# Kernel tuning notes

Hardware: AMD Instinct MI355X
Metric: run time of the kernel (lower is better)

Reference implementation:

```python
import jax, jax.numpy as jnp
import numpy as np

N, D = 4096, 512
TAU, ALPHA, BETA = 0.8, 0.55, 0.4
ADJ_P = 0.005  # sparse binary adjacency density (avg degree ~20)


def setup_inputs() -> dict:
    key = jax.random.key(0)
    ks = jax.random.split(key, 8)
    z1 = jax.random.normal(ks[0], (N, D), dtype=jnp.float32)
    z2 = jax.random.normal(ks[1], (N, D), dtype=jnp.float32)

    def adj(k):
        a = jax.random.bernoulli(k, ADJ_P, (N, N)).astype(jnp.float32)
        # adjacency masks are binary {0,1}; zero the diagonal like the model does
        return a * (1.0 - jnp.eye(N, dtype=jnp.float32))

    return {
        "z1": z1,
        "z2": z2,
        "adj_c": adj(ks[2]),
        "adj_m": adj(ks[3]),
        "adj_f": adj(ks[4]),
        "adj_c_aug": adj(ks[5]),
        "adj_m_aug": adj(ks[6]),
        "adj_f_aug": adj(ks[7]),
    }


def _normalize(z):
    # F.normalize(z, dim=1): divide by L2 norm clamped at 1e-12
    n = jnp.maximum(jnp.linalg.norm(z, axis=1, keepdims=True), 1e-12)
    return z / n


def _cl_loss(z, z_aug, adj, tau):
    zn = _normalize(z)
    zan = _normalize(z_aug)
    intra = jnp.exp((zn @ zn.T) / tau)          # [N, N]
    inter = jnp.exp((zn @ zan.T) / tau)         # [N, N]
    intra_diag = jnp.diagonal(intra)
    positive = jnp.diagonal(inter) + (intra * adj).sum(1) + (inter * adj).sum(1)
    denom = intra.sum(1) + inter.sum(1) - intra_diag
    adj_count = adj.sum(1) * 2.0 + 1.0
    loss = jnp.log(positive / denom) / adj_count
    return -jnp.mean(loss)


def _final_cl_loss(z, z_aug, adj, adj_aug, tau):
    return ALPHA * _cl_loss(z, z_aug, adj, tau) + BETA * _cl_loss(z_aug, z, adj_aug, tau)


def reference(z1, z2, adj_c, adj_m, adj_f, adj_c_aug, adj_m_aug, adj_f_aug):
    loss_coarse = _final_cl_loss(z1, z2, adj_c, adj_c_aug, TAU)
    loss_medium = _final_cl_loss(z1, z2, adj_m, adj_m_aug, TAU)
    loss_fine = _final_cl_loss(z1, z2, adj_f, adj_f_aug, TAU)
    loss_cross_cf = _final_cl_loss(z1, z2, adj_c, adj_f_aug, TAU * 0.8)
    loss_cross_mf = _final_cl_loss(z1, z2, adj_m, adj_f_aug, TAU * 0.9)

    sc, sm, sf = adj_c.sum(), adj_m.sum(), adj_f.sum()
    total_info = sc + sm + sf + 1e-08
    scale_loss = (sc / total_info) * loss_coarse + (sm / total_info) * loss_medium + (sf / total_info) * loss_fine
    cross_loss = 0.2 * (loss_cross_cf + loss_cross_mf)
    return scale_loss + cross_loss
```

## Files before the change

### kernel.cpp

```cpp
#include <hip/hip_runtime.h>
#include <hip/hip_bf16.h>

#define NR 4096
#define DD 512
#define CAP 64

typedef __bf16 bf16x8 __attribute__((ext_vector_type(8)));
typedef float f32x4 __attribute__((ext_vector_type(4)));
typedef unsigned short u16;

#define AS_GLOBAL(p) ((const __attribute__((address_space(1))) unsigned int*)(p))
#define AS_LDS(p)    ((__attribute__((address_space(3))) unsigned int*)(p))

__device__ __forceinline__ u16 f2bf(float x) {
    __hip_bfloat16 h = __float2bfloat16(x);
    return *reinterpret_cast<u16*>(&h);
}

__device__ __forceinline__ float blo(unsigned u) { return __uint_as_float(u << 16); }
__device__ __forceinline__ float bhi(unsigned u) { return __uint_as_float(u & 0xffff0000u); }

__global__ void norm_kernel(const float* z1, const float* z2,
                            u16* zn1, u16* zn2, float* d12) {
    const int row = blockIdx.x;
    const int t = threadIdx.x;
    const float* r1 = z1 + (size_t)row * DD;
    const float* r2 = z2 + (size_t)row * DD;
    float a0 = r1[t], a1 = r1[t + 256];
    float b0 = r2[t], b1 = r2[t + 256];
    float ss1 = a0 * a0 + a1 * a1;
    float ss2 = b0 * b0 + b1 * b1;
    #pragma unroll
    for (int m = 1; m < 64; m <<= 1) {
        ss1 += __shfl_xor(ss1, m);
        ss2 += __shfl_xor(ss2, m);
    }
    __shared__ float s1s[4], s2s[4], ds[4];
    const int wid = t >> 6, lane = t & 63;
    if (lane == 0) { s1s[wid] = ss1; s2s[wid] = ss2; }
    __syncthreads();
    const float n1 = s1s[0] + s1s[1] + s1s[2] + s1s[3];
    const float n2 = s2s[0] + s2s[1] + s2s[2] + s2s[3];
    const float inv1 = 1.0f / fmaxf(sqrtf(n1), 1e-12f);
    const float inv2 = 1.0f / fmaxf(sqrtf(n2), 1e-12f);
    const float u0 = a0 * inv1, u1 = a1 * inv1;
    const float v0 = b0 * inv2, v1 = b1 * inv2;
    zn1[(size_t)row * DD + t]       = f2bf(u0);
    zn1[(size_t)row * DD + t + 256] = f2bf(u1);
    zn2[(size_t)row * DD + t]       = f2bf(v0);
    zn2[(size_t)row * DD + t + 256] = f2bf(v1);
    float dp = u0 * v0 + u1 * v1;
    #pragma unroll
    for (int m = 1; m < 64; m <<= 1) dp += __shfl_xor(dp, m);
    if (lane == 0) ds[wid] = dp;
    __syncthreads();
    if (t == 0) d12[row] = ds[0] + ds[1] + ds[2] + ds[3];
}

__global__ __launch_bounds__(256)
void sparsify_kernel(const float* m0, const float* m1, const float* m2,
                     const float* m3, const float* m4, const float* m5,
                     int* cnts, int* idx, float* asum) {
    const int row = blockIdx.x;
    const int m = blockIdx.y;
    const int t = threadIdx.x;
    const float* M = (m == 0) ? m0 : (m == 1) ? m1 : (m == 2) ? m2
                   : (m == 3) ? m3 : (m == 4) ? m4 : m5;
    const float* rowp = M + (size_t)row * NR;
    __shared__ int s_cnt;
    __shared__ int s_idx[CAP];
    if (t == 0) s_cnt = 0;
    __syncthreads();
    #pragma unroll
    for (int q = 0; q < 4; q++) {
        const int vi = t + 256 * q;
        const float4 v = ((const float4*)rowp)[vi];
        const int col = vi * 4;
        if (v.x != 0.f) { int p = atomicAdd(&s_cnt, 1); if (p < CAP) s_idx[p] = col; }
        if (v.y != 0.f) { int p = atomicAdd(&s_cnt, 1); if (p < CAP) s_idx[p] = col + 1; }
        if (v.z != 0.f) { int p = atomicAdd(&s_cnt, 1); if (p < CAP) s_idx[p] = col + 2; }
        if (v.w != 0.f) { int p = atomicAdd(&s_cnt, 1); if (p < CAP) s_idx[p] = col + 3; }
    }
    __syncthreads();
    const int c = min(s_cnt, CAP);
    const size_t base = (size_t)m * NR + row;
    if (t < c) idx[base * CAP + t] = s_idx[t];
    if (t == 0) { cnts[base] = c; asum[base] = (float)s_cnt; }
}

__global__ __launch_bounds__(256, 3)
void score_kernel(const u16* __restrict__ zn1, const u16* __restrict__ zn2,
                  float* __restrict__ part) {
    int id = blockIdx.x;
    int mode, by, bx;
    if (id < 1024) {
        mode = 1; by = id >> 5; bx = id & 31;
    } else {
        int k = id - 1024;
        mode = 0;
        if (k >= 528) { k -= 528; mode = 2; }
        int v = (int)((65.0f - sqrtf(4225.0f - 8.0f * (float)k)) * 0.5f);
        if (v < 0) v = 0; if (v > 31) v = 31;
        while (v < 31 && (v + 1) * 32 - ((v + 1) * v) / 2 <= k) v++;
        while (v > 0 && v * 32 - (v * (v - 1)) / 2 > k) v--;
        by = v;
        bx = by + (k - (by * 32 - (by * (by - 1)) / 2));
    }
    const int Ib = by * 128, Jb = bx * 128;
    const u16* Ag = (mode == 2) ? zn2 : zn1;
    const u16* Bg = (mode == 0) ? zn1 : zn2;
    const int p_row = mode;
    const int p_col = (mode == 1) ? 3 : mode;
    const bool do_cols = (mode == 1) || (bx != by);

    __shared__ u16 As[128 * 64];
    __shared__ u16 Bs[128 * 64];
    __shared__ float sRow[2][3][128];
    __shared__ float sCol[2][3][128];

    const int tid = threadIdx.x;
    const int lane = tid & 63;
    const int wid = tid >> 6;
    const int wm = wid >> 1, wn = wid & 1;
    const int quad = lane >> 4, lcol = lane & 15;

    f32x4 acc[4][4];
    #pragma unroll
    for (int a = 0; a < 4; a++)
        #pragma unroll
        for (int b = 0; b < 4; b++)
            acc[a][b] = (f32x4){0.f, 0.f, 0.f, 0.f};

    size_t gA[4], gB[4];
    unsigned ldsoff[4];
    #pragma unroll
    for (int cc = 0; cc < 4; cc++) {
        const int ch = cc * 4 + wid;
        const int p = ch * 64 + lane;
        const int r = p >> 3;
        const int kb = (p & 7) ^ (r & 7);
        ldsoff[cc] = (unsigned)ch * 1024u;
        gA[cc] = (size_t)(Ib + r) * DD + kb * 8;
        gB[cc] = (size_t)(Jb + r) * DD + kb * 8;
    }

    for (int k0 = 0; k0 < DD; k0 += 64) {
        __syncthreads();
        #pragma unroll
        for (int cc = 0; cc < 4; cc++) {
            __builtin_amdgcn_global_load_lds(AS_GLOBAL(Ag + gA[cc] + k0),
                                             AS_LDS((char*)As + ldsoff[cc]), 16, 0, 0);
            __builtin_amdgcn_global_load_lds(AS_GLOBAL(Bg + gB[cc] + k0),
                                             AS_LDS((char*)Bs + ldsoff[cc]), 16, 0, 0);
        }
        __syncthreads();
        #pragma unroll
        for (int kk = 0; kk < 64; kk += 32) {
            const int kbb = (kk >> 3) + quad;
            bf16x8 a[4], b[4];
            #pragma unroll
            for (int i = 0; i < 4; i++) {
                const int ra = wm * 64 + i * 16 + lcol;
                const int rb = wn * 64 + i * 16 + lcol;
                a[i] = *(const bf16x8*)&As[ra * 64 + ((kbb ^ (ra & 7)) * 8)];
                b[i] = *(const bf16x8*)&Bs[rb * 64 + ((kbb ^ (rb & 7)) * 8)];
            }
            #pragma unroll
            for (int mi = 0; mi < 4; mi++)
                #pragma unroll
                for (int ni = 0; ni < 4; ni++)
                    acc[mi][ni] = __builtin_amdgcn_mfma_f32_16x16x32_bf16(a[mi], b[ni], acc[mi][ni], 0, 0, 0);
        }
    }

    const float C0 = 1.8033688011112042f;
    const float C1 = 2.2542110013890054f;
    const float C2 = 2.0037431123457825f;

    float colacc[3][4];
    #pragma unroll
    for (int t = 0; t < 3; t++)
        #pragma unroll
        for (int ni = 0; ni < 4; ni++) colacc[t][ni] = 0.f;

    #pragma unroll
    for (int mi = 0; mi < 4; mi++) {
        #pragma unroll
        for (int reg = 0; reg < 4; reg++) {
            float p0 = 0.f, p1 = 0.f, p2 = 0.f;
            #pragma unroll
            for (int ni = 0; ni < 4; ni++) {
                const float s = acc[mi][ni][reg];
                const float e0 = __builtin_amdgcn_exp2f(s * C0);
                const float e1 = __builtin_amdgcn_exp2f(s * C1);
                const float e2 = __builtin_amdgcn_exp2f(s * C2);
                p0 += e0; p1 += e1; p2 += e2;
                colacc[0][ni] += e0; colacc[1][ni] += e1; colacc[2][ni] += e2;
            }
            p0 += __shfl_xor(p0, 1); p0 += __shfl_xor(p0, 2); p0 += __shfl_xor(p0, 4); p0 += __shfl_xor(p0, 8);
            p1 += __shfl_xor(p1, 1); p1 += __shfl_xor(p1, 2); p1 += __shfl_xor(p1, 4); p1 += __shfl_xor(p1, 8);
            p2 += __shfl_xor(p2, 1); p2 += __shfl_xor(p2, 2); p2 += __shfl_xor(p2, 4); p2 += __shfl_xor(p2, 8);
            if (lcol == 0) {
                const int r = wm * 64 + mi * 16 + quad * 4 + reg;
                sRow[wn][0][r] = p0; sRow[wn][1][r] = p1; sRow[wn][2][r] = p2;
            }
        }
    }
    #pragma unroll
    for (int t = 0; t < 3; t++) {
        #pragma unroll
        for (int ni = 0; ni < 4; ni++) {
            float v = colacc[t][ni];
            v += __shfl_xor(v, 16); v += __shfl_xor(v, 32);
            if (quad == 0) sCol[wm][t][wn * 64 + ni * 16 + lcol] = v;
        }
    }
    __syncthreads();
    if (tid < 128) {
        const int i = Ib + tid;
        #pragma unroll
        for (int t = 0; t < 3; t++) {
            const float v = sRow[0][t][tid] + sRow[1][t][tid];
            part[(((size_t)p_row * 3 + t) * 32 + bx) * NR + i] = v;
        }
    } else if (do_cols) {
        const int c = tid - 128;
        const int i = Jb + c;
        #pragma unroll
        for (int t = 0; t < 3; t++) {
            const float v = sCol[0][t][c] + sCol[1][t][c];
            part[(((size_t)p_col * 3 + t) * 32 + by) * NR + i] = v;
        }
    }
}

__global__ __launch_bounds__(256)
void reduce_kernel(const float* __restrict__ part, float* __restrict__ rs) {
    const int g = blockIdx.x * 256 + threadIdx.x;
    const int pt = g >> 12;
    const int i = g & (NR - 1);
    const float* base = part + ((size_t)pt * 32) * NR + i;
    float s = 0.f;
    #pragma unroll
    for (int k = 0; k < 32; k++) s += base[(size_t)k * NR];
    rs[(size_t)pt * NR + i] = s;
}

__global__ __launch_bounds__(256)
void sparse_kernel(const u16* __restrict__ zn1, const u16* __restrict__ zn2,
                   const int* __restrict__ cnts, const int* __restrict__ idx,
                   float* __restrict__ ms) {
    const int w = blockIdx.x * 4 + (threadIdx.x >> 6);
    const int lane = threadIdx.x & 63;
    const int g = lane >> 4;
    const int l = lane & 15;
    const int m = w >> 12;
    const int i = w & (NR - 1);

    const float C0 = 1.8033688011112042f;
    const float C1 = 2.2542110013890054f;
    const float C2 = 2.0037431123457825f;

    int nslot; int slot[3]; float coef[3];
    switch (m) {
        case 0: nslot = 2; slot[0] = 0; coef[0] = C0; slot[1] = 3; coef[1] = C1; break;
        case 1: nslot = 2; slot[0] = 1; coef[0] = C0; slot[1] = 4; coef[1] = C2; break;
        case 2: nslot = 1; slot[0] = 2; coef[0] = C0; break;
        case 3: nslot = 1; slot[0] = 0; coef[0] = C0; break;
        case 4: nslot = 1; slot[0] = 1; coef[0] = C0; break;
        default: nslot = 3; slot[0] = 2; coef[0] = C0; slot[1] = 3; coef[1] = C1;
                 slot[2] = 4; coef[2] = C2; break;
    }

    const u16* A = (m < 3) ? zn1 : zn2;
    float a[32];
    {
        const uint4* ap = (const uint4*)(A + (size_t)i * DD) + l * 4;
        #pragma unroll
        for (int t = 0; t < 4; t++) {
            const uint4 r = ap[t];
            const unsigned* u = (const unsigned*)&r;
            #pragma unroll
            for (int q = 0; q < 4; q++) {
                a[t * 8 + 2 * q]     = blo(u[q]);
                a[t * 8 + 2 * q + 1] = bhi(u[q]);
            }
        }
    }

    const size_t base = (size_t)m * NR + i;
    const int cnt = cnts[base];
    const int* ji = idx + base * CAP;
    const int jreg = ji[(lane < cnt) ? lane : (cnt > 0 ? cnt - 1 : 0)];

    float acc[3][2] = {{0.f, 0.f}, {0.f, 0.f}, {0.f, 0.f}};

    for (int q0 = 0; q0 < cnt; q0 += 8) {
        const int qa = q0 + g;
        const int qb = qa + 4;
        const bool va = qa < cnt;
        const bool vb = qb < cnt;
        const int ja = __shfl(jreg, va ? qa : 0);
        const int jb = __shfl(jreg, vb ? qb : 0);

        const uint4* p1a = (const uint4*)(zn1 + (size_t)ja * DD) + l * 4;
        const uint4* p2a = (const uint4*)(zn2 + (size_t)ja * DD) + l * 4;
        const uint4* p1b = (const uint4*)(zn1 + (size_t)jb * DD) + l * 4;
        const uint4* p2b = (const uint4*)(zn2 + (size_t)jb * DD) + l * 4;
        uint4 r1a[4], r2a[4], r1b[4], r2b[4];
        #pragma unroll
        for (int t = 0; t < 4; t++) {
            r1a[t] = p1a[t]; r2a[t] = p2a[t];
            r1b[t] = p1b[t]; r2b[t] = p2b[t];
        }

        float s1a0 = 0.f, s1a1 = 0.f, s2a0 = 0.f, s2a1 = 0.f;
        float s1b0 = 0.f, s1b1 = 0.f, s2b0 = 0.f, s2b1 = 0.f;
        #pragma unroll
        for (int t = 0; t < 4; t++) {
            const unsigned* u1a = (const unsigned*)&r1a[t];
            const unsigned* u2a = (const unsigned*)&r2a[t];
            const unsigned* u1b = (const unsigned*)&r1b[t];
            const unsigned* u2b = (const unsigned*)&r2b[t];
            #pragma unroll
            for (int q = 0; q < 4; q++) {
                const float alo = a[t * 8 + 2 * q], ahi = a[t * 8 + 2 * q + 1];
                s1a0 += alo * blo(u1a[q]); s1a1 += ahi * bhi(u1a[q]);
                s2a0 += alo * blo(u2a[q]); s2a1 += ahi * bhi(u2a[q]);
                s1b0 += alo * blo(u1b[q]); s1b1 += ahi * bhi(u1b[q]);
                s2b0 += alo * blo(u2b[q]); s2b1 += ahi * bhi(u2b[q]);
            }
        }
        float d1a = s1a0 + s1a1, d2a = s2a0 + s2a1;
        float d1b = s1b0 + s1b1, d2b = s2b0 + s2b1;

        #pragma unroll
        for (int msk = 1; msk < 16; msk <<= 1) {
            d1a += __shfl_xor(d1a, msk); d2a += __shfl_xor(d2a, msk);
            d1b += __shfl_xor(d1b, msk); d2b += __shfl_xor(d2b, msk);
        }

        const float e1a = (m < 3) ? d1a : d2a, e2a = (m < 3) ? d2a : d1a;
        const float e1b = (m < 3) ? d1b : d2b, e2b = (m < 3) ? d2b : d1b;
        if (va) {
            for (int s = 0; s < nslot; s++) {
                acc[s][0] += __builtin_amdgcn_exp2f(e1a * coef[s]);
                acc[s][1] += __builtin_amdgcn_exp2f(e2a * coef[s]);
            }
        }
        if (vb) {
            for (int s = 0; s < nslot; s++) {
                acc[s][0] += __builtin_amdgcn_exp2f(e1b * coef[s]);
                acc[s][1] += __builtin_amdgcn_exp2f(e2b * coef[s]);
            }
        }
    }

    #pragma unroll
    for (int s = 0; s < 3; s++) {
        #pragma unroll
        for (int h = 0; h < 2; h++) {
            float v = acc[s][h];
            v += __shfl_xor(v, 16);
            v += __shfl_xor(v, 32);
            acc[s][h] = v;
        }
    }
    if (lane == 0) {
        const int pb = (m < 3) ? 0 : 2;
        for (int s = 0; s < nslot; s++) {
            ms[((pb)     * 5 + slot[s]) * NR + i] = acc[s][0];
            ms[((pb + 1) * 5 + slot[s]) * NR + i] = acc[s][1];
        }
    }
}

__global__ void finalize_kernel(const float* rs, const float* ms, const float* asum,
                                const float* d12, float* out) {
    const int t = threadIdx.x;
    const int tA[5] = {0, 0, 0, 1, 2};
    const int kA[5] = {0, 1, 2, 3, 4};
    const int aA[5] = {0, 1, 2, 0, 1};
    const int aB[5] = {3, 4, 5, 5, 5};
    const float it[3] = {1.25f, 1.5625f, 1.3888888888888888f};
    const float e1t[3] = {expf(1.25f), expf(1.5625f), expf(1.3888888888888888f)};

    float LA[5] = {0, 0, 0, 0, 0}, LB[5] = {0, 0, 0, 0, 0};
    float sc = 0.f, sm = 0.f, sf = 0.f;

    for (int i = t; i < NR; i += 256) {
        const float d = d12[i];
        float ed[3];
        ed[0] = __expf(d * it[0]); ed[1] = __expf(d * it[1]); ed[2] = __expf(d * it[2]);
        float R[4][3], M[4][5], A6[6];
        #pragma unroll
        for (int p = 0; p < 4; p++) {
            #pragma unroll
            for (int tt = 0; tt < 3; tt++) R[p][tt] = rs[(p * 3 + tt) * NR + i];
            #pragma unroll
            for (int k = 0; k < 5; k++) M[p][k] = ms[(p * 5 + k) * NR + i];
        }
        #pragma unroll
        for (int a = 0; a < 6; a++) A6[a] = asum[a * NR + i];

        #pragma unroll
        for (int c = 0; c < 5; c++) {
            const int tt = tA[c], k = kA[c];
            float pos = ed[tt] + M[0][k] + M[1][k];
            float den = R[0][tt] + R[1][tt] - e1t[tt];
            float cnt = 2.f * A6[aA[c]] + 1.f;
            LA[c] += __logf(pos / den) / cnt;
            pos = ed[tt] + M[2][k] + M[3][k];
            den = R[2][tt] + R[3][tt] - e1t[tt];
            cnt = 2.f * A6[aB[c]] + 1.f;
            LB[c] += __logf(pos / den) / cnt;
        }
        sc += A6[0]; sm += A6[1]; sf += A6[2];
    }

    __shared__ float red[256];
    float vals[13] = {LA[0], LA[1], LA[2], LA[3], LA[4],
                      LB[0], LB[1], LB[2], LB[3], LB[4], sc, sm, sf};
    __shared__ float tot[13];
    for (int q = 0; q < 13; q++) {
        red[t] = vals[q];
        __syncthreads();
        for (int s = 128; s > 0; s >>= 1) {
            if (t < s) red[t] += red[t + s];
            __syncthreads();
        }
        if (t == 0) tot[q] = red[0];
        __syncthreads();
    }
    if (t == 0) {
        float Ac[5], Bc[5];
        #pragma unroll
        for (int c = 0; c < 5; c++) {
            Ac[c] = -tot[c] / (float)NR;
            Bc[c] = -tot[5 + c] / (float)NR;
        }
        const float ALPHA = 0.55f, BETA = 0.4f;
        const float Lc  = ALPHA * Ac[0] + BETA * Bc[0];
        const float Lm  = ALPHA * Ac[1] + BETA * Bc[1];
        const float Lf  = ALPHA * Ac[2] + BETA * Bc[2];
        const float Lcf = ALPHA * Ac[3] + BETA * Bc[3];
        const float Lmf = ALPHA * Ac[4] + BETA * Bc[4];
        const float scs = tot[10], sms = tot[11], sfs = tot[12];
        const float tot_info = scs + sms + sfs + 1e-8f;
        out[0] = (scs * Lc + sms * Lm + sfs * Lf) / tot_info + 0.2f * (Lcf + Lmf);
    }
}

extern "C" void kernel_launch(void* const* d_in, const int* in_sizes, int n_in,
                              void* d_out, int out_size, void* d_ws, size_t ws_size,
                              hipStream_t stream) {
    const float* z1  = (const float*)d_in[0];
    const float* z2  = (const float*)d_in[1];
    const float* ac  = (const float*)d_in[2];
    const float* am  = (const float*)d_in[3];
    const float* af  = (const float*)d_in[4];
    const float* aca = (const float*)d_in[5];
    const float* ama = (const float*)d_in[6];
    const float* afa = (const float*)d_in[7];

    float* ws   = (float*)d_ws;
    float* rs   = ws;
    float* ms   = rs + 12 * NR;
    float* asum = ms + 20 * NR;
    float* d12  = asum + 6 * NR;
    u16* zn1 = (u16*)(d12 + NR);
    u16* zn2 = zn1 + (size_t)NR * DD;
    int* cnts = (int*)(zn2 + (size_t)NR * DD);
    int* idx  = cnts + 6 * NR;
    float* part = (float*)(idx + (size_t)6 * NR * CAP);

    norm_kernel<<<NR, 256, 0, stream>>>(z1, z2, zn1, zn2, d12);
    dim3 sg(NR, 6);
    sparsify_kernel<<<sg, 256, 0, stream>>>(ac, am, af, aca, ama, afa, cnts, idx, asum);
    score_kernel<<<1024 + 2 * 528, 256, 0, stream>>>(zn1, zn2, part);
    sparse_kernel<<<6 * NR / 4, 256, 0, stream>>>(zn1, zn2, cnts, idx, ms);
    reduce_kernel<<<12 * NR / 256, 256, 0, stream>>>(part, rs);
    finalize_kernel<<<1, 256, 0, stream>>>(rs, ms, asum, d12, (float*)d_out);
}
```

Measured before the change: 585.5 us.

## Fuse dense score and sparse neighbor kernels; wave-per-row sparsify with ballot-free scan

```diff
diff --git a/kernel.cpp b/kernel.cpp
--- a/kernel.cpp
+++ b/kernel.cpp
@@ -61,175 +61,315 @@
 void sparsify_kernel(const float* m0, const float* m1, const float* m2,
                      const float* m3, const float* m4, const float* m5,
                      int* cnts, int* idx, float* asum) {
-    const int row = blockIdx.x;
-    const int m = blockIdx.y;
-    const int t = threadIdx.x;
+    const int w = blockIdx.x * 4 + (threadIdx.x >> 6);
+    const int lane = threadIdx.x & 63;
+    const int m = w >> 12;
+    const int row = w & (NR - 1);
     const float* M = (m == 0) ? m0 : (m == 1) ? m1 : (m == 2) ? m2
                    : (m == 3) ? m3 : (m == 4) ? m4 : m5;
-    const float* rowp = M + (size_t)row * NR;
-    __shared__ int s_cnt;
-    __shared__ int s_idx[CAP];
-    if (t == 0) s_cnt = 0;
-    __syncthreads();
+    const float4* p = (const float4*)(M + (size_t)row * NR) + lane;
+
+    unsigned long long mask = 0ull;
     #pragma unroll
-    for (int q = 0; q < 4; q++) {
-        const int vi = t + 256 * q;
-        const float4 v = ((const float4*)rowp)[vi];
-        const int col = vi * 4;
-        if (v.x != 0.f) { int p = atomicAdd(&s_cnt, 1); if (p < CAP) s_idx[p] = col; }
-        if (v.y != 0.f) { int p = atomicAdd(&s_cnt, 1); if (p < CAP) s_idx[p] = col + 1; }
-        if (v.z != 0.f) { int p = atomicAdd(&s_cnt, 1); if (p < CAP) s_idx[p] = col + 2; }
-        if (v.w != 0.f) { int p = atomicAdd(&s_cnt, 1); if (p < CAP) s_idx[p] = col + 3; }
-    }
-    __syncthreads();
-    const int c = min(s_cnt, CAP);
+    for (int t = 0; t < 16; t++) {
+        const float4 v = p[t * 64];
+        mask |= (unsigned long long)((v.x != 0.f ? 1u : 0u)
+               | (v.y != 0.f ? 2u : 0u)
+               | (v.z != 0.f ? 4u : 0u)
+               | (v.w != 0.f ? 8u : 0u)) << (t * 4);
+    }
+    const int n = __popcll(mask);
+    int off = n;
+    #pragma unroll
+    for (int d = 1; d < 64; d <<= 1) {
+        const int tu = __shfl_up(off, d);
+        if (lane >= d) off += tu;
+    }
+    const int total = __shfl(off, 63);
+    int pos = off - n;
     const size_t base = (size_t)m * NR + row;
-    if (t < c) idx[base * CAP + t] = s_idx[t];
-    if (t == 0) { cnts[base] = c; asum[base] = (float)s_cnt; }
-}
-
-__global__ __launch_bounds__(256, 3)
-void score_kernel(const u16* __restrict__ zn1, const u16* __restrict__ zn2,
-                  float* __restrict__ part) {
-    int id = blockIdx.x;
-    int mode, by, bx;
-    if (id < 1024) {
-        mode = 1; by = id >> 5; bx = id & 31;
-    } else {
-        int k = id - 1024;
-        mode = 0;
-        if (k >= 528) { k -= 528; mode = 2; }
-        int v = (int)((65.0f - sqrtf(4225.0f - 8.0f * (float)k)) * 0.5f);
-        if (v < 0) v = 0; if (v > 31) v = 31;
-        while (v < 31 && (v + 1) * 32 - ((v + 1) * v) / 2 <= k) v++;
-        while (v > 0 && v * 32 - (v * (v - 1)) / 2 > k) v--;
-        by = v;
-        bx = by + (k - (by * 32 - (by * (by - 1)) / 2));
-    }
-    const int Ib = by * 128, Jb = bx * 128;
-    const u16* Ag = (mode == 2) ? zn2 : zn1;
-    const u16* Bg = (mode == 0) ? zn1 : zn2;
-    const int p_row = mode;
-    const int p_col = (mode == 1) ? 3 : mode;
-    const bool do_cols = (mode == 1) || (bx != by);
-
+    unsigned long long mm = mask;
+    while (mm) {
+        const int b = __ffsll(mm) - 1;
+        mm &= mm - 1;
+        const int t = b >> 2, j = b & 3;
+        if (pos < CAP) idx[base * CAP + pos] = (t * 64 + lane) * 4 + j;
+        pos++;
+    }
+    if (lane == 63) {
+        cnts[base] = min(total, CAP);
+        asum[base] = (float)total;
+    }
+}
+
+__global__ __launch_bounds__(256, 4)
+void fused_kernel(const u16* __restrict__ zn1, const u16* __restrict__ zn2,
+                  const int* __restrict__ cnts, const int* __restrict__ idx,
+                  float* __restrict__ part, float* __restrict__ ms) {
     __shared__ u16 As[128 * 64];
     __shared__ u16 Bs[128 * 64];
     __shared__ float sRow[2][3][128];
     __shared__ float sCol[2][3][128];
 
+    const int bid = blockIdx.x;
     const int tid = threadIdx.x;
     const int lane = tid & 63;
-    const int wid = tid >> 6;
-    const int wm = wid >> 1, wn = wid & 1;
-    const int quad = lane >> 4, lcol = lane & 15;
-
-    f32x4 acc[4][4];
-    #pragma unroll
-    for (int a = 0; a < 4; a++)
-        #pragma unroll
-        for (int b = 0; b < 4; b++)
-            acc[a][b] = (f32x4){0.f, 0.f, 0.f, 0.f};
-
-    size_t gA[4], gB[4];
-    unsigned ldsoff[4];
-    #pragma unroll
-    for (int cc = 0; cc < 4; cc++) {
-        const int ch = cc * 4 + wid;
-        const int p = ch * 64 + lane;
-        const int r = p >> 3;
-        const int kb = (p & 7) ^ (r & 7);
-        ldsoff[cc] = (unsigned)ch * 1024u;
-        gA[cc] = (size_t)(Ib + r) * DD + kb * 8;
-        gB[cc] = (size_t)(Jb + r) * DD + kb * 8;
-    }
-
-    for (int k0 = 0; k0 < DD; k0 += 64) {
-        __syncthreads();
-        #pragma unroll
-        for (int cc = 0; cc < 4; cc++) {
-            __builtin_amdgcn_global_load_lds(AS_GLOBAL(Ag + gA[cc] + k0),
-                                             AS_LDS((char*)As + ldsoff[cc]), 16, 0, 0);
-            __builtin_amdgcn_global_load_lds(AS_GLOBAL(Bg + gB[cc] + k0),
-                                             AS_LDS((char*)Bs + ldsoff[cc]), 16, 0, 0);
-        }
-        __syncthreads();
-        #pragma unroll
-        for (int kk = 0; kk < 64; kk += 32) {
-            const int kbb = (kk >> 3) + quad;
-            bf16x8 a[4], b[4];
-            #pragma unroll
-            for (int i = 0; i < 4; i++) {
-                const int ra = wm * 64 + i * 16 + lcol;
-                const int rb = wn * 64 + i * 16 + lcol;
-                a[i] = *(const bf16x8*)&As[ra * 64 + ((kbb ^ (ra & 7)) * 8)];
-                b[i] = *(const bf16x8*)&Bs[rb * 64 + ((kbb ^ (rb & 7)) * 8)];
-            }
-            #pragma unroll
-            for (int mi = 0; mi < 4; mi++)
-                #pragma unroll
-                for (int ni = 0; ni < 4; ni++)
-                    acc[mi][ni] = __builtin_amdgcn_mfma_f32_16x16x32_bf16(a[mi], b[ni], acc[mi][ni], 0, 0, 0);
-        }
-    }
 
     const float C0 = 1.8033688011112042f;
     const float C1 = 2.2542110013890054f;
     const float C2 = 2.0037431123457825f;
 
-    float colacc[3][4];
-    #pragma unroll
-    for (int t = 0; t < 3; t++)
-        #pragma unroll
-        for (int ni = 0; ni < 4; ni++) colacc[t][ni] = 0.f;
-
-    #pragma unroll
-    for (int mi = 0; mi < 4; mi++) {
-        #pragma unroll
-        for (int reg = 0; reg < 4; reg++) {
-            float p0 = 0.f, p1 = 0.f, p2 = 0.f;
+    if ((bid & 3) == 0) {
+        int id = bid >> 2;
+        int mode, by, bx;
+        if (id < 1024) {
+            mode = 1; by = id >> 5; bx = id & 31;
+        } else {
+            int k = id - 1024;
+            mode = 0;
+            if (k >= 528) { k -= 528; mode = 2; }
+            int v = (int)((65.0f - sqrtf(4225.0f - 8.0f * (float)k)) * 0.5f);
+            if (v < 0) v = 0; if (v > 31) v = 31;
+            while (v < 31 && (v + 1) * 32 - ((v + 1) * v) / 2 <= k) v++;
+            while (v > 0 && v * 32 - (v * (v - 1)) / 2 > k) v--;
+            by = v;
+            bx = by + (k - (by * 32 - (by * (by - 1)) / 2));
+        }
+        const int Ib = by * 128, Jb = bx * 128;
+        const u16* Ag = (mode == 2) ? zn2 : zn1;
+        const u16* Bg = (mode == 0) ? zn1 : zn2;
+        const int p_row = mode;
+        const int p_col = (mode == 1) ? 3 : mode;
+        const bool do_cols = (mode == 1) || (bx != by);
+
+        const int wid = tid >> 6;
+        const int wm = wid >> 1, wn = wid & 1;
+        const int quad = lane >> 4, lcol = lane & 15;
+
+        f32x4 acc[4][4];
+        #pragma unroll
+        for (int a = 0; a < 4; a++)
+            #pragma unroll
+            for (int b = 0; b < 4; b++)
+                acc[a][b] = (f32x4){0.f, 0.f, 0.f, 0.f};
+
+        size_t gA[4], gB[4];
+        unsigned ldsoff[4];
+        #pragma unroll
+        for (int cc = 0; cc < 4; cc++) {
+            const int ch = cc * 4 + wid;
+            const int p = ch * 64 + lane;
+            const int r = p >> 3;
+            const int kb = (p & 7) ^ (r & 7);
+            ldsoff[cc] = (unsigned)ch * 1024u;
+            gA[cc] = (size_t)(Ib + r) * DD + kb * 8;
+            gB[cc] = (size_t)(Jb + r) * DD + kb * 8;
+        }
+
+        for (int k0 = 0; k0 < DD; k0 += 64) {
+            __syncthreads();
+            #pragma unroll
+            for (int cc = 0; cc < 4; cc++) {
+                __builtin_amdgcn_global_load_lds(AS_GLOBAL(Ag + gA[cc] + k0),
+                                                 AS_LDS((char*)As + ldsoff[cc]), 16, 0, 0);
+                __builtin_amdgcn_global_load_lds(AS_GLOBAL(Bg + gB[cc] + k0),
+                                                 AS_LDS((char*)Bs + ldsoff[cc]), 16, 0, 0);
+            }
+            __syncthreads();
+            #pragma unroll
+            for (int kk = 0; kk < 64; kk += 32) {
+                const int kbb = (kk >> 3) + quad;
+                bf16x8 a[4], b[4];
+                #pragma unroll
+                for (int i = 0; i < 4; i++) {
+                    const int ra = wm * 64 + i * 16 + lcol;
+                    const int rb = wn * 64 + i * 16 + lcol;
+                    a[i] = *(const bf16x8*)&As[ra * 64 + ((kbb ^ (ra & 7)) * 8)];
+                    b[i] = *(const bf16x8*)&Bs[rb * 64 + ((kbb ^ (rb & 7)) * 8)];
+                }
+                #pragma unroll
+                for (int mi = 0; mi < 4; mi++)
+                    #pragma unroll
+                    for (int ni = 0; ni < 4; ni++)
+                        acc[mi][ni] = __builtin_amdgcn_mfma_f32_16x16x32_bf16(a[mi], b[ni], acc[mi][ni], 0, 0, 0);
+            }
+        }
+
+        float colacc[3][4];
+        #pragma unroll
+        for (int t = 0; t < 3; t++)
+            #pragma unroll
+            for (int ni = 0; ni < 4; ni++) colacc[t][ni] = 0.f;
+
+        #pragma unroll
+        for (int mi = 0; mi < 4; mi++) {
+            #pragma unroll
+            for (int reg = 0; reg < 4; reg++) {
+                float p0 = 0.f, p1 = 0.f, p2 = 0.f;
+                #pragma unroll
+                for (int ni = 0; ni < 4; ni++) {
+                    const float s = acc[mi][ni][reg];
+                    const float e0 = __builtin_amdgcn_exp2f(s * C0);
+                    const float e1 = __builtin_amdgcn_exp2f(s * C1);
+                    const float e2 = __builtin_amdgcn_exp2f(s * C2);
+                    p0 += e0; p1 += e1; p2 += e2;
+                    colacc[0][ni] += e0; colacc[1][ni] += e1; colacc[2][ni] += e2;
+                }
+                p0 += __shfl_xor(p0, 1); p0 += __shfl_xor(p0, 2); p0 += __shfl_xor(p0, 4); p0 += __shfl_xor(p0, 8);
+                p1 += __shfl_xor(p1, 1); p1 += __shfl_xor(p1, 2); p1 += __shfl_xor(p1, 4); p1 += __shfl_xor(p1, 8);
+                p2 += __shfl_xor(p2, 1); p2 += __shfl_xor(p2, 2); p2 += __shfl_xor(p2, 4); p2 += __shfl_xor(p2, 8);
+                if (lcol == 0) {
+                    const int r = wm * 64 + mi * 16 + quad * 4 + reg;
+                    sRow[wn][0][r] = p0; sRow[wn][1][r] = p1; sRow[wn][2][r] = p2;
+                }
+            }
+        }
+        #pragma unroll
+        for (int t = 0; t < 3; t++) {
             #pragma unroll
             for (int ni = 0; ni < 4; ni++) {
-                const float s = acc[mi][ni][reg];
-                const float e0 = __builtin_amdgcn_exp2f(s * C0);
-                const float e1 = __builtin_amdgcn_exp2f(s * C1);
-                const float e2 = __builtin_amdgcn_exp2f(s * C2);
-                p0 += e0; p1 += e1; p2 += e2;
-                colacc[0][ni] += e0; colacc[1][ni] += e1; colacc[2][ni] += e2;
-            }
-            p0 += __shfl_xor(p0, 1); p0 += __shfl_xor(p0, 2); p0 += __shfl_xor(p0, 4); p0 += __shfl_xor(p0, 8);
-            p1 += __shfl_xor(p1, 1); p1 += __shfl_xor(p1, 2); p1 += __shfl_xor(p1, 4); p1 += __shfl_xor(p1, 8);
-            p2 += __shfl_xor(p2, 1); p2 += __shfl_xor(p2, 2); p2 += __shfl_xor(p2, 4); p2 += __shfl_xor(p2, 8);
-            if (lcol == 0) {
-                const int r = wm * 64 + mi * 16 + quad * 4 + reg;
-                sRow[wn][0][r] = p0; sRow[wn][1][r] = p1; sRow[wn][2][r] = p2;
-            }
-        }
-    }
-    #pragma unroll
-    for (int t = 0; t < 3; t++) {
-        #pragma unroll
-        for (int ni = 0; ni < 4; ni++) {
-            float v = colacc[t][ni];
-            v += __shfl_xor(v, 16); v += __shfl_xor(v, 32);
-            if (quad == 0) sCol[wm][t][wn * 64 + ni * 16 + lcol] = v;
-        }
-    }
-    __syncthreads();
-    if (tid < 128) {
-        const int i = Ib + tid;
-        #pragma unroll
-        for (int t = 0; t < 3; t++) {
-            const float v = sRow[0][t][tid] + sRow[1][t][tid];
-            part[(((size_t)p_row * 3 + t) * 32 + bx) * NR + i] = v;
-        }
-    } else if (do_cols) {
-        const int c = tid - 128;
-        const int i = Jb + c;
-        #pragma unroll
-        for (int t = 0; t < 3; t++) {
-            const float v = sCol[0][t][c] + sCol[1][t][c];
-            part[(((size_t)p_col * 3 + t) * 32 + by) * NR + i] = v;
+                float v = colacc[t][ni];
+                v += __shfl_xor(v, 16); v += __shfl_xor(v, 32);
+                if (quad == 0) sCol[wm][t][wn * 64 + ni * 16 + lcol] = v;
+            }
+        }
+        __syncthreads();
+        if (tid < 128) {
+            const int i = Ib + tid;
+            #pragma unroll
+            for (int t = 0; t < 3; t++) {
+                const float v = sRow[0][t][tid] + sRow[1][t][tid];
+                part[(((size_t)p_row * 3 + t) * 32 + bx) * NR + i] = v;
+            }
+        } else if (do_cols) {
+            const int c = tid - 128;
+            const int i = Jb + c;
+            #pragma unroll
+            for (int t = 0; t < 3; t++) {
+                const float v = sCol[0][t][c] + sCol[1][t][c];
+                part[(((size_t)p_col * 3 + t) * 32 + by) * NR + i] = v;
+            }
+        }
+    } else {
+        const int sid = bid - (bid >> 2) - 1;
+        if (sid >= 6144) return;
+        const int w = sid * 4 + (tid >> 6);
+        const int g = lane >> 4;
+        const int l = lane & 15;
+        const int m = w >> 12;
+        const int i = w & (NR - 1);
+
+        int nslot; int slot[3]; float coef[3];
+        switch (m) {
+            case 0: nslot = 2; slot[0] = 0; coef[0] = C0; slot[1] = 3; coef[1] = C1; break;
+            case 1: nslot = 2; slot[0] = 1; coef[0] = C0; slot[1] = 4; coef[1] = C2; break;
+            case 2: nslot = 1; slot[0] = 2; coef[0] = C0; break;
+            case 3: nslot = 1; slot[0] = 0; coef[0] = C0; break;
+            case 4: nslot = 1; slot[0] = 1; coef[0] = C0; break;
+            default: nslot = 3; slot[0] = 2; coef[0] = C0; slot[1] = 3; coef[1] = C1;
+                     slot[2] = 4; coef[2] = C2; break;
+        }
+
+        const u16* A = (m < 3) ? zn1 : zn2;
+        float a[32];
+        {
+            const uint4* ap = (const uint4*)(A + (size_t)i * DD) + l * 4;
+            #pragma unroll
+            for (int t = 0; t < 4; t++) {
+                const uint4 r = ap[t];
+                const unsigned* u = (const unsigned*)&r;
+                #pragma unroll
+                for (int q = 0; q < 4; q++) {
+                    a[t * 8 + 2 * q]     = blo(u[q]);
+                    a[t * 8 + 2 * q + 1] = bhi(u[q]);
+                }
+            }
+        }
+
+        const size_t base = (size_t)m * NR + i;
+        const int cnt = cnts[base];
+        const int* ji = idx + base * CAP;
+        const int jreg = ji[(lane < cnt) ? lane : (cnt > 0 ? cnt - 1 : 0)];
+
+        float acc[3][2] = {{0.f, 0.f}, {0.f, 0.f}, {0.f, 0.f}};
+
+        for (int q0 = 0; q0 < cnt; q0 += 8) {
+            const int qa = q0 + g;
+            const int qb = qa + 4;
+            const bool va = qa < cnt;
+            const bool vb = qb < cnt;
+            const int ja = __shfl(jreg, va ? qa : 0);
+            const int jb = __shfl(jreg, vb ? qb : 0);
+
+            const uint4* p1a = (const uint4*)(zn1 + (size_t)ja * DD) + l * 4;
+            const uint4* p2a = (const uint4*)(zn2 + (size_t)ja * DD) + l * 4;
+            const uint4* p1b = (const uint4*)(zn1 + (size_t)jb * DD) + l * 4;
+            const uint4* p2b = (const uint4*)(zn2 + (size_t)jb * DD) + l * 4;
+            uint4 r1a[4], r2a[4], r1b[4], r2b[4];
+            #pragma unroll
+            for (int t = 0; t < 4; t++) {
+                r1a[t] = p1a[t]; r2a[t] = p2a[t];
+                r1b[t] = p1b[t]; r2b[t] = p2b[t];
+            }
+
+            float s1a0 = 0.f, s1a1 = 0.f, s2a0 = 0.f, s2a1 = 0.f;
+            float s1b0 = 0.f, s1b1 = 0.f, s2b0 = 0.f, s2b1 = 0.f;
+            #pragma unroll
+            for (int t = 0; t < 4; t++) {
+                const unsigned* u1a = (const unsigned*)&r1a[t];
+                const unsigned* u2a = (const unsigned*)&r2a[t];
+                const unsigned* u1b = (const unsigned*)&r1b[t];
+                const unsigned* u2b = (const unsigned*)&r2b[t];
+                #pragma unroll
+                for (int q = 0; q < 4; q++) {
+                    const float alo = a[t * 8 + 2 * q], ahi = a[t * 8 + 2 * q + 1];
+                    s1a0 += alo * blo(u1a[q]); s1a1 += ahi * bhi(u1a[q]);
+                    s2a0 += alo * blo(u2a[q]); s2a1 += ahi * bhi(u2a[q]);
+                    s1b0 += alo * blo(u1b[q]); s1b1 += ahi * bhi(u1b[q]);
+                    s2b0 += alo * blo(u2b[q]); s2b1 += ahi * bhi(u2b[q]);
+                }
+            }
+            float d1a = s1a0 + s1a1, d2a = s2a0 + s2a1;
+            float d1b = s1b0 + s1b1, d2b = s2b0 + s2b1;
+
+            #pragma unroll
+            for (int msk = 1; msk < 16; msk <<= 1) {
+                d1a += __shfl_xor(d1a, msk); d2a += __shfl_xor(d2a, msk);
+                d1b += __shfl_xor(d1b, msk); d2b += __shfl_xor(d2b, msk);
+            }
+
+            const float e1a = (m < 3) ? d1a : d2a, e2a = (m < 3) ? d2a : d1a;
+            const float e1b = (m < 3) ? d1b : d2b, e2b = (m < 3) ? d2b : d1b;
+            if (va) {
+                for (int s = 0; s < nslot; s++) {
+                    acc[s][0] += __builtin_amdgcn_exp2f(e1a * coef[s]);
+                    acc[s][1] += __builtin_amdgcn_exp2f(e2a * coef[s]);
+                }
+            }
+            if (vb) {
+                for (int s = 0; s < nslot; s++) {
+                    acc[s][0] += __builtin_amdgcn_exp2f(e1b * coef[s]);
+                    acc[s][1] += __builtin_amdgcn_exp2f(e2b * coef[s]);
+                }
+            }
+        }
+
+        #pragma unroll
+        for (int s = 0; s < 3; s++) {
+            #pragma unroll
+            for (int h = 0; h < 2; h++) {
+                float v = acc[s][h];
+                v += __shfl_xor(v, 16);
+                v += __shfl_xor(v, 32);
+                acc[s][h] = v;
+            }
+        }
+        if (lane == 0) {
+            const int pb = (m < 3) ? 0 : 2;
+            for (int s = 0; s < nslot; s++) {
+                ms[((pb)     * 5 + slot[s]) * NR + i] = acc[s][0];
+                ms[((pb + 1) * 5 + slot[s]) * NR + i] = acc[s][1];
+            }
         }
     }
 }
@@ -244,135 +384,6 @@
     #pragma unroll
     for (int k = 0; k < 32; k++) s += base[(size_t)k * NR];
     rs[(size_t)pt * NR + i] = s;
-}
-
-__global__ __launch_bounds__(256)
-void sparse_kernel(const u16* __restrict__ zn1, const u16* __restrict__ zn2,
-                   const int* __restrict__ cnts, const int* __restrict__ idx,
-                   float* __restrict__ ms) {
-    const int w = blockIdx.x * 4 + (threadIdx.x >> 6);
-    const int lane = threadIdx.x & 63;
-    const int g = lane >> 4;
-    const int l = lane & 15;
-    const int m = w >> 12;
-    const int i = w & (NR - 1);
-
-    const float C0 = 1.8033688011112042f;
-    const float C1 = 2.2542110013890054f;
-    const float C2 = 2.0037431123457825f;
-
-    int nslot; int slot[3]; float coef[3];
-    switch (m) {
-        case 0: nslot = 2; slot[0] = 0; coef[0] = C0; slot[1] = 3; coef[1] = C1; break;
-        case 1: nslot = 2; slot[0] = 1; coef[0] = C0; slot[1] = 4; coef[1] = C2; break;
-        case 2: nslot = 1; slot[0] = 2; coef[0] = C0; break;
-        case 3: nslot = 1; slot[0] = 0; coef[0] = C0; break;
-        case 4: nslot = 1; slot[0] = 1; coef[0] = C0; break;
-        default: nslot = 3; slot[0] = 2; coef[0] = C0; slot[1] = 3; coef[1] = C1;
-                 slot[2] = 4; coef[2] = C2; break;
-    }
-
-    const u16* A = (m < 3) ? zn1 : zn2;
-    float a[32];
-    {
-        const uint4* ap = (const uint4*)(A + (size_t)i * DD) + l * 4;
-        #pragma unroll
-        for (int t = 0; t < 4; t++) {
-            const uint4 r = ap[t];
-            const unsigned* u = (const unsigned*)&r;
-            #pragma unroll
-            for (int q = 0; q < 4; q++) {
-                a[t * 8 + 2 * q]     = blo(u[q]);
-                a[t * 8 + 2 * q + 1] = bhi(u[q]);
-            }
-        }
-    }
-
-    const size_t base = (size_t)m * NR + i;
-    const int cnt = cnts[base];
-    const int* ji = idx + base * CAP;
-    const int jreg = ji[(lane < cnt) ? lane : (cnt > 0 ? cnt - 1 : 0)];
-
-    float acc[3][2] = {{0.f, 0.f}, {0.f, 0.f}, {0.f, 0.f}};
-
-    for (int q0 = 0; q0 < cnt; q0 += 8) {
-        const int qa = q0 + g;
-        const int qb = qa + 4;
-        const bool va = qa < cnt;
-        const bool vb = qb < cnt;
-        const int ja = __shfl(jreg, va ? qa : 0);
-        const int jb = __shfl(jreg, vb ? qb : 0);
-
-        const uint4* p1a = (const uint4*)(zn1 + (size_t)ja * DD) + l * 4;
-        const uint4* p2a = (const uint4*)(zn2 + (size_t)ja * DD) + l * 4;
-        const uint4* p1b = (const uint4*)(zn1 + (size_t)jb * DD) + l * 4;
-        const uint4* p2b = (const uint4*)(zn2 + (size_t)jb * DD) + l * 4;
-        uint4 r1a[4], r2a[4], r1b[4], r2b[4];
-        #pragma unroll
-        for (int t = 0; t < 4; t++) {
-            r1a[t] = p1a[t]; r2a[t] = p2a[t];
-            r1b[t] = p1b[t]; r2b[t] = p2b[t];
-        }
-
-        float s1a0 = 0.f, s1a1 = 0.f, s2a0 = 0.f, s2a1 = 0.f;
-        float s1b0 = 0.f, s1b1 = 0.f, s2b0 = 0.f, s2b1 = 0.f;
-        #pragma unroll
-        for (int t = 0; t < 4; t++) {
-            const unsigned* u1a = (const unsigned*)&r1a[t];
-            const unsigned* u2a = (const unsigned*)&r2a[t];
-            const unsigned* u1b = (const unsigned*)&r1b[t];
-            const unsigned* u2b = (const unsigned*)&r2b[t];
-            #pragma unroll
-            for (int q = 0; q < 4; q++) {
-                const float alo = a[t * 8 + 2 * q], ahi = a[t * 8 + 2 * q + 1];
-                s1a0 += alo * blo(u1a[q]); s1a1 += ahi * bhi(u1a[q]);
-                s2a0 += alo * blo(u2a[q]); s2a1 += ahi * bhi(u2a[q]);
-                s1b0 += alo * blo(u1b[q]); s1b1 += ahi * bhi(u1b[q]);
-                s2b0 += alo * blo(u2b[q]); s2b1 += ahi * bhi(u2b[q]);
-            }
-        }
-        float d1a = s1a0 + s1a1, d2a = s2a0 + s2a1;
-        float d1b = s1b0 + s1b1, d2b = s2b0 + s2b1;
-
-        #pragma unroll
-        for (int msk = 1; msk < 16; msk <<= 1) {
-            d1a += __shfl_xor(d1a, msk); d2a += __shfl_xor(d2a, msk);
-            d1b += __shfl_xor(d1b, msk); d2b += __shfl_xor(d2b, msk);
-        }
-
-        const float e1a = (m < 3) ? d1a : d2a, e2a = (m < 3) ? d2a : d1a;
-        const float e1b = (m < 3) ? d1b : d2b, e2b = (m < 3) ? d2b : d1b;
-        if (va) {
-            for (int s = 0; s < nslot; s++) {
-                acc[s][0] += __builtin_amdgcn_exp2f(e1a * coef[s]);
-                acc[s][1] += __builtin_amdgcn_exp2f(e2a * coef[s]);
-            }
-        }
-        if (vb) {
-            for (int s = 0; s < nslot; s++) {
-                acc[s][0] += __builtin_amdgcn_exp2f(e1b * coef[s]);
-                acc[s][1] += __builtin_amdgcn_exp2f(e2b * coef[s]);
-            }
-        }
-    }
-
-    #pragma unroll
-    for (int s = 0; s < 3; s++) {
-        #pragma unroll
-        for (int h = 0; h < 2; h++) {
-            float v = acc[s][h];
-            v += __shfl_xor(v, 16);
-            v += __shfl_xor(v, 32);
-            acc[s][h] = v;
-        }
-    }
-    if (lane == 0) {
-        const int pb = (m < 3) ? 0 : 2;
-        for (int s = 0; s < nslot; s++) {
-            ms[((pb)     * 5 + slot[s]) * NR + i] = acc[s][0];
-            ms[((pb + 1) * 5 + slot[s]) * NR + i] = acc[s][1];
-        }
-    }
 }
 
 __global__ void finalize_kernel(const float* rs, const float* ms, const float* asum,
@@ -475,10 +486,8 @@
     float* part = (float*)(idx + (size_t)6 * NR * CAP);
 
     norm_kernel<<<NR, 256, 0, stream>>>(z1, z2, zn1, zn2, d12);
-    dim3 sg(NR, 6);
-    sparsify_kernel<<<sg, 256, 0, stream>>>(ac, am, af, aca, ama, afa, cnts, idx, asum);
-    score_kernel<<<1024 + 2 * 528, 256, 0, stream>>>(zn1, zn2, part);
-    sparse_kernel<<<6 * NR / 4, 256, 0, stream>>>(zn1, zn2, cnts, idx, ms);
+    sparsify_kernel<<<6 * NR / 4, 256, 0, stream>>>(ac, am, af, aca, ama, afa, cnts, idx, asum);
+    fused_kernel<<<8320, 256, 0, stream>>>(zn1, zn2, cnts, idx, part, ms);
     reduce_kernel<<<12 * NR / 256, 256, 0, stream>>>(part, rs);
     finalize_kernel<<<1, 256, 0, stream>>>(rs, ms, asum, d12, (float*)d_out);
 }
```

New measurement: 752.8 us. 1.29x slower.
